# Performance work log

Measured on AMD Instinct MI355X. Metric: run time of the kernel, lower is better.

The kernel has to match this reference:

```python
import jax, jax.numpy as jnp
import numpy as np

B, S, DIM = 2, 2048, 2048
N_HEADS, N_KV_HEADS = 16, 4
HEAD_DIM = DIM // N_HEADS  # 128
N_REP = N_HEADS // N_KV_HEADS  # 4
ROPE_THETA = 10000.0


def setup_inputs() -> dict:
    key = jax.random.key(0)
    ks = jax.random.split(key, 6)
    x = jax.random.normal(ks[0], (B, S, DIM), dtype=jnp.float32)
    # torch nn.Linear weights are [out_features, in_features]
    sc = 0.02
    wq = jax.random.normal(ks[1], (N_HEADS * HEAD_DIM, DIM), dtype=jnp.float32) * sc
    wk = jax.random.normal(ks[2], (N_KV_HEADS * HEAD_DIM, DIM), dtype=jnp.float32) * sc
    wv = jax.random.normal(ks[3], (N_KV_HEADS * HEAD_DIM, DIM), dtype=jnp.float32) * sc
    wo = jax.random.normal(ks[4], (DIM, N_HEADS * HEAD_DIM), dtype=jnp.float32) * sc
    # precomputed rotary table (freqs_cis in llama): [S, head_dim//2]
    inv_freq = 1.0 / (ROPE_THETA ** (jnp.arange(0, HEAD_DIM, 2, dtype=jnp.float32) / HEAD_DIM))
    t = jnp.arange(S, dtype=jnp.float32)
    freqs = jnp.outer(t, inv_freq)  # [S, head_dim//2]
    freqs_cos = jnp.cos(freqs)
    freqs_sin = jnp.sin(freqs)
    # additive causal mask as passed to SDPA (float, 0 on allowed, -inf-like elsewhere)
    causal = jnp.tril(jnp.ones((S, S), dtype=bool))
    mask = jnp.where(causal, 0.0, -1e9).astype(jnp.float32)
    return {"x": x, "wq": wq, "wk": wk, "wv": wv, "wo": wo,
            "freqs_cos": freqs_cos, "freqs_sin": freqs_sin, "mask": mask}


def _apply_rope(t, cos, sin):
    # t: [B, S, H, D]; cos/sin: [S, D//2] -> complex multiply on adjacent pairs
    tr = t.reshape(*t.shape[:-1], -1, 2)  # [B,S,H,D/2,2]
    tre, tim = tr[..., 0], tr[..., 1]
    c = cos[None, :, None, :]
    s = sin[None, :, None, :]
    out_re = tre * c - tim * s
    out_im = tre * s + tim * c
    return jnp.stack([out_re, out_im], axis=-1).reshape(t.shape)


def reference(x, wq, wk, wv, wo, freqs_cos, freqs_sin, mask):
    Bx, Sx, _ = x.shape
    xq = (x @ wq.T).reshape(Bx, Sx, N_HEADS, HEAD_DIM)
    xk = (x @ wk.T).reshape(Bx, Sx, N_KV_HEADS, HEAD_DIM)
    xv = (x @ wv.T).reshape(Bx, Sx, N_KV_HEADS, HEAD_DIM)
    xq = _apply_rope(xq, freqs_cos, freqs_sin)
    xk = _apply_rope(xk, freqs_cos, freqs_sin)
    # repeat_kv for GQA: [B,S,KV,D] -> [B,S,KV*n_rep,D]
    keys = jnp.repeat(xk, N_REP, axis=2)
    values = jnp.repeat(xv, N_REP, axis=2)
    q = xq.transpose(0, 2, 1, 3)      # [B,H,S,D]
    k = keys.transpose(0, 2, 1, 3)
    v = values.transpose(0, 2, 1, 3)
    scale = 1.0 / jnp.sqrt(jnp.float32(HEAD_DIM))
    scores = jnp.einsum('bhqd,bhkd->bhqk', q, k) * scale + mask[None, None]
    attn = jax.nn.softmax(scores, axis=-1)
    out = jnp.einsum('bhqk,bhkd->bhqd', attn, v)
    out = out.transpose(0, 2, 1, 3).reshape(Bx, Sx, -1)
    return out @ wo.T
```

## Files before the change

kernel.cpp:

```cpp
#include <hip/hip_runtime.h>
#include <hip/hip_bf16.h>

#define B_   2
#define S_   2048
#define DIM_ 2048
#define NH   16
#define NKV  4
#define HD   128
#define QKVN 3072

typedef __attribute__((ext_vector_type(8)))  short  sv8;
typedef __attribute__((ext_vector_type(8)))  ushort usv8;
typedef __attribute__((ext_vector_type(4)))  float  fv4;
typedef __attribute__((ext_vector_type(16))) float  fv16;

__device__ __forceinline__ float fast_exp2(float x) {
  return __builtin_amdgcn_exp2f(x);
}

__device__ __forceinline__ ushort f2bf(float f) {
  __hip_bfloat16 h = __float2bfloat16(f);
  union { __hip_bfloat16 h; ushort u; } c; c.h = h; return c.u;
}
__device__ __forceinline__ float bf2f(ushort u) {
  union { unsigned int i; float f; } c; c.i = ((unsigned)u) << 16; return c.f;
}

__device__ __forceinline__ unsigned int cvtpk(float lo, float hi) {
  unsigned int r;
  asm("v_cvt_pk_bf16_f32 %0, %1, %2" : "=v"(r) : "v"(lo), "v"(hi));
  return r;
}
__device__ __forceinline__ unsigned int xhalf(unsigned int x) {
  return (unsigned int)__shfl_xor((int)x, 32, 64);
}

__device__ __forceinline__ void async16(const void* g, void* l) {
  __builtin_amdgcn_global_load_lds(
      (const __attribute__((address_space(1))) unsigned int*)g,
      (__attribute__((address_space(3))) unsigned int*)l, 16, 0, 0);
}

__global__ void cvt_kernel(const float* __restrict__ in, ushort* __restrict__ out, int n) {
  int i = (blockIdx.x * 256 + threadIdx.x) * 4;
  if (i >= n) return;
  fv4 v = *(const fv4*)(in + i);
  ushort4 o;
  o.x = f2bf(v[0]); o.y = f2bf(v[1]); o.z = f2bf(v[2]); o.w = f2bf(v[3]);
  *(ushort4*)(out + i) = o;
}

__global__ void rope_kernel(const ushort* __restrict__ raw, const float* __restrict__ fc,
                            const float* __restrict__ fs, ushort* __restrict__ out,
                            int heads, int rowstride, float scale) {
  int t = blockIdx.x * 256 + threadIdx.x;
  int grp = t & 15;
  int h   = (t >> 4) % heads;
  int s   = ((t >> 4) / heads) % S_;
  int b   = t / (16 * heads * S_);
  const ushort* src = raw + (size_t)(b * S_ + s) * rowstride + h * HD + grp * 8;
  sv8 v = *(const sv8*)src;
  fv4 c  = *(const fv4*)(fc + s * 64 + grp * 4);
  fv4 sn = *(const fv4*)(fs + s * 64 + grp * 4);
  sv8 o;
#pragma unroll
  for (int p = 0; p < 4; ++p) {
    float re = bf2f((ushort)v[2 * p]);
    float im = bf2f((ushort)v[2 * p + 1]);
    float orr = (re * c[p] - im * sn[p]) * scale;
    float oi  = (re * sn[p] + im * c[p]) * scale;
    o[2 * p]     = (short)f2bf(orr);
    o[2 * p + 1] = (short)f2bf(oi);
  }
  ushort* dst = out + ((size_t)(b * heads + h) * S_ + s) * HD + grp * 8;
  *(sv8*)dst = o;
}

__global__ __launch_bounds__(256) void vtrans_kernel(const ushort* __restrict__ vraw,
                                                     ushort* __restrict__ vt, int rowstride) {
  __shared__ ushort tile[128][136];
  int blk = blockIdx.x;
  int st  = blk & 15;
  int kvb = blk >> 4;
  int kv  = kvb & 3;
  int b   = kvb >> 2;
  int s0  = st << 7;
#pragma unroll
  for (int it = 0; it < 8; ++it) {
    int t = it * 256 + threadIdx.x;
    int srow = t >> 4;
    int d8 = (t & 15) * 8;
    usv8 v = *(const usv8*)(vraw + (size_t)(b * S_ + s0 + srow) * rowstride + kv * HD + d8);
#pragma unroll
    for (int j = 0; j < 8; ++j) tile[d8 + j][srow] = v[j];
  }
  __syncthreads();
#pragma unroll
  for (int it = 0; it < 8; ++it) {
    int t = it * 256 + threadIdx.x;
    int d = t >> 4;
    int s8 = (t & 15) * 8;
    usv8 o;
#pragma unroll
    for (int j = 0; j < 8; ++j) o[j] = tile[d][s8 + j];
    *(usv8*)(vt + ((size_t)(b * NKV + kv) * HD + d) * S_ + s0 + s8) = o;
  }
}

template <typename OutT>
__global__ __launch_bounds__(256) void gemm_bt(const ushort* __restrict__ A,
                                               const ushort* __restrict__ Bm,
                                               OutT* __restrict__ C,
                                               int M, int N, int K) {
  __shared__ ushort As[128 * 64];
  __shared__ ushort Bs[128 * 64];
  int nb = N >> 7;
  int bx = blockIdx.x % nb;
  int by = blockIdx.x / nb;
  int m0 = by << 7, n0 = bx << 7;
  int lane = threadIdx.x & 63, w = threadIdx.x >> 6;
  int l15 = lane & 15, lg = lane >> 4;
  int wm = (w >> 1) * 64, wn = (w & 1) * 64;

  const ushort* aSrc[4]; const ushort* bSrc[4];
  ushort* aDst[4]; ushort* bDst[4];
#pragma unroll
  for (int it = 0; it < 4; ++it) {
    int lin = it * 4096 + w * 1024 + lane * 16;
    int row = lin >> 7;
    int cb  = (lin & 127) ^ ((row & 7) << 4);
    aSrc[it] = A  + (size_t)(m0 + row) * K + (cb >> 1);
    bSrc[it] = Bm + (size_t)(n0 + row) * K + (cb >> 1);
    aDst[it] = As + ((it * 4096 + w * 1024) >> 1);
    bDst[it] = Bs + ((it * 4096 + w * 1024) >> 1);
  }

  fv4 acc[4][4] = {};

  for (int kt = 0; kt < K; kt += 64) {
#pragma unroll
    for (int it = 0; it < 4; ++it) async16(aSrc[it] + kt, aDst[it]);
#pragma unroll
    for (int it = 0; it < 4; ++it) async16(bSrc[it] + kt, bDst[it]);
    __syncthreads();
#pragma unroll
    for (int kk = 0; kk < 2; ++kk) {
      sv8 af[4], bfr[4];
#pragma unroll
      for (int i = 0; i < 4; ++i) {
        int row = wm + i * 16 + l15;
        int byt = row * 128 + ((kk * 64 + (lg << 4)) ^ ((row & 7) << 4));
        af[i] = *(const sv8*)((const char*)As + byt);
      }
#pragma unroll
      for (int j = 0; j < 4; ++j) {
        int row = wn + j * 16 + l15;
        int byt = row * 128 + ((kk * 64 + (lg << 4)) ^ ((row & 7) << 4));
        bfr[j] = *(const sv8*)((const char*)Bs + byt);
      }
#pragma unroll
      for (int i = 0; i < 4; ++i)
#pragma unroll
        for (int j = 0; j < 4; ++j)
          acc[i][j] = __builtin_amdgcn_mfma_f32_16x16x32_bf16(af[i], bfr[j], acc[i][j], 0, 0, 0);
    }
    __syncthreads();
  }

#pragma unroll
  for (int i = 0; i < 4; ++i)
#pragma unroll
    for (int j = 0; j < 4; ++j)
#pragma unroll
      for (int r = 0; r < 4; ++r) {
        int row = m0 + wm + i * 16 + (lg << 2) + r;
        int col = n0 + wn + j * 16 + l15;
        if constexpr (sizeof(OutT) == 2) C[(size_t)row * N + col] = (OutT)f2bf(acc[i][j][r]);
        else                             C[(size_t)row * N + col] = (OutT)acc[i][j][r];
      }
}

__global__ __launch_bounds__(256, 2) void attn_kernel(const ushort* __restrict__ Q,
                                                      const ushort* __restrict__ Kr,
                                                      const ushort* __restrict__ Vt,
                                                      ushort* __restrict__ O) {
  __shared__ ushort Ks[2][64 * 128];
  __shared__ ushort Vs[2][128 * 64];

  int blk = blockIdx.x;
  int bh  = blk & 31;
  int idx = blk >> 5;
  int qt  = (idx & 1) ? (idx >> 1) : (15 - (idx >> 1));
  int h   = bh & 15;
  int b   = bh >> 4;
  int kv  = h >> 2;
  int q0  = qt << 7;
  int lane = threadIdx.x & 63, w = threadIdx.x >> 6;
  int l31 = lane & 31, hh = lane >> 5;
  int qrow_w = q0 + w * 32;
  int myq    = qrow_w + l31;

  const ushort* Qbase = Q  + (size_t)(b * NH  + h ) * S_ * HD;
  const ushort* Kbase = Kr + (size_t)(b * NKV + kv) * S_ * HD;
  const ushort* Vbase = Vt + (size_t)(b * NKV + kv) * HD * S_;

  sv8 qf[8];
#pragma unroll
  for (int kk = 0; kk < 8; ++kk)
    qf[kk] = *(const sv8*)(Qbase + (size_t)myq * HD + kk * 16 + hh * 8);

  const ushort* kSrc[4]; ushort* kDst[4];
  const ushort* vSrc[4]; ushort* vDst[4];
#pragma unroll
  for (int it = 0; it < 4; ++it) {
    int lin = it * 4096 + w * 1024 + lane * 16;
    { int row = lin >> 8; int cb = (lin & 255) ^ ((row & 7) << 4);
      kSrc[it] = Kbase + (size_t)row * HD + (cb >> 1);
      kDst[it] = Ks[0] + ((it * 4096 + w * 1024) >> 1); }
    { int row = lin >> 7; int cb = (lin & 127) ^ ((row & 7) << 4);
      vSrc[it] = Vbase + (size_t)row * S_ + (cb >> 1);
      vDst[it] = Vs[0] + ((it * 4096 + w * 1024) >> 1); }
  }

  fv16 oacc[4] = {};
  float mrun = -1e30f, lrun = 0.f;

  int nkt = (q0 >> 6) + 2;

#pragma unroll
  for (int it = 0; it < 4; ++it) async16(kSrc[it], kDst[it]);
#pragma unroll
  for (int it = 0; it < 4; ++it) async16(vSrc[it], vDst[it]);

  for (int kt = 0; kt < nkt; ++kt) {
    int cur = kt & 1, nxt = cur ^ 1;
    __syncthreads();
    if (kt + 1 < nkt) {
      size_t k0n = (size_t)(kt + 1) << 6;
#pragma unroll
      for (int it = 0; it < 4; ++it) async16(kSrc[it] + k0n * HD, kDst[it] + nxt * (64 * 128));
#pragma unroll
      for (int it = 0; it < 4; ++it) async16(vSrc[it] + k0n,      vDst[it] + nxt * (128 * 64));
    }
    const char* KsC = (const char*)Ks[cur];
    const char* VsC = (const char*)Vs[cur];
    int k0 = kt << 6;

    fv16 sacc[2] = {};
    __builtin_amdgcn_s_setprio(1);
#pragma unroll
    for (int kk = 0; kk < 8; ++kk) {
      int cb = kk * 32 + hh * 16;
      int r0 = l31, r1 = 32 + l31;
      sv8 kf0 = *(const sv8*)(KsC + r0 * 256 + (cb ^ ((r0 & 7) << 4)));
      sv8 kf1 = *(const sv8*)(KsC + r1 * 256 + (cb ^ ((r1 & 7) << 4)));
      sacc[0] = __builtin_amdgcn_mfma_f32_32x32x16_bf16(kf0, qf[kk], sacc[0], 0, 0, 0);
      sacc[1] = __builtin_amdgcn_mfma_f32_32x32x16_bf16(kf1, qf[kk], sacc[1], 0, 0, 0);
    }
    __builtin_amdgcn_s_setprio(0);

    if (k0 + 63 > qrow_w) {
      int thr = myq - k0 - 4 * hh;
#pragma unroll
      for (int t = 0; t < 2; ++t)
#pragma unroll
        for (int r = 0; r < 16; ++r) {
          int kp = t * 32 + (r & 3) + 8 * (r >> 2);
          if (kp > thr) sacc[t][r] = -1e30f;
        }
    }

    float tmax = sacc[0][0];
#pragma unroll
    for (int t = 0; t < 2; ++t)
#pragma unroll
      for (int r = 0; r < 16; ++r) tmax = fmaxf(tmax, sacc[t][r]);
    tmax = fmaxf(tmax, __shfl_xor(tmax, 32, 64));

    if (__any(tmax > mrun + 8.0f)) {
      float mnew = fmaxf(mrun, tmax);
      float esc  = fast_exp2(mrun - mnew);
      lrun *= esc;
      float er[16];
#pragma unroll
      for (int r = 0; r < 16; ++r) er[r] = __shfl(esc, (r & 3) + 8 * (r >> 2) + 4 * hh, 64);
#pragma unroll
      for (int d0 = 0; d0 < 4; ++d0)
#pragma unroll
        for (int r = 0; r < 16; ++r) oacc[d0][r] *= er[r];
      mrun = mnew;
    }

    float psum = 0.f;
#pragma unroll
    for (int t = 0; t < 2; ++t)
#pragma unroll
      for (int r = 0; r < 16; ++r) {
        float p = fast_exp2(sacc[t][r] - mrun);
        sacc[t][r] = p;
        psum += p;
      }
    psum += __shfl_xor(psum, 32, 64);
    lrun += psum;

    union Frag { unsigned int u[4]; sv8 v; } pa[4];
#pragma unroll
    for (int t = 0; t < 2; ++t)
#pragma unroll
      for (int half = 0; half < 2; ++half) {
        int cb = half * 8;
        unsigned int a0 = cvtpk(sacc[t][cb + 0], sacc[t][cb + 1]);
        unsigned int a1 = cvtpk(sacc[t][cb + 2], sacc[t][cb + 3]);
        unsigned int b0 = cvtpk(sacc[t][cb + 4], sacc[t][cb + 5]);
        unsigned int b1 = cvtpk(sacc[t][cb + 6], sacc[t][cb + 7]);
        unsigned int a0p = xhalf(a0), a1p = xhalf(a1);
        unsigned int b0p = xhalf(b0), b1p = xhalf(b1);
        pa[2 * t + half].u[0] = hh ? b0p : a0;
        pa[2 * t + half].u[1] = hh ? b1p : a1;
        pa[2 * t + half].u[2] = hh ? b0  : a0p;
        pa[2 * t + half].u[3] = hh ? b1  : a1p;
      }

    __builtin_amdgcn_s_setprio(1);
#pragma unroll
    for (int ks = 0; ks < 4; ++ks) {
      int cb = ks * 32 + hh * 16;
#pragma unroll
      for (int d0 = 0; d0 < 4; ++d0) {
        int row = d0 * 32 + l31;
        sv8 vf = *(const sv8*)(VsC + row * 128 + (cb ^ ((row & 7) << 4)));
        oacc[d0] = __builtin_amdgcn_mfma_f32_32x32x16_bf16(pa[ks].v, vf, oacc[d0], 0, 0, 0);
      }
    }
    __builtin_amdgcn_s_setprio(0);
  }

  float inv = 1.0f / lrun;
  float ir[16];
#pragma unroll
  for (int r = 0; r < 16; ++r) ir[r] = __shfl(inv, (r & 3) + 8 * (r >> 2) + 4 * hh, 64);
#pragma unroll
  for (int r = 0; r < 16; ++r) {
    int q = qrow_w + (r & 3) + 8 * (r >> 2) + 4 * hh;
#pragma unroll
    for (int d0 = 0; d0 < 4; ++d0) {
      int d = d0 * 32 + l31;
      O[(size_t)(b * S_ + q) * DIM_ + h * HD + d] = f2bf(oacc[d0][r] * ir[r]);
    }
  }
}

extern "C" void kernel_launch(void* const* d_in, const int* in_sizes, int n_in,
                              void* d_out, int out_size, void* d_ws, size_t ws_size,
                              hipStream_t stream) {
  const float* x  = (const float*)d_in[0];
  const float* wq = (const float*)d_in[1];
  const float* wk = (const float*)d_in[2];
  const float* wv = (const float*)d_in[3];
  const float* wo = (const float*)d_in[4];
  const float* fc = (const float*)d_in[5];
  const float* fs = (const float*)d_in[6];
  float* out = (float*)d_out;

  char* ws = (char*)d_ws;
  size_t off = 0;
  auto alloc = [&](size_t bytes) -> ushort* {
    ushort* p = (ushort*)(ws + off);
    off += (bytes + 255) & ~(size_t)255;
    return p;
  };
  ushort* xb    = alloc((size_t)B_ * S_ * DIM_ * 2);
  ushort* wqkvb = alloc((size_t)QKVN * DIM_ * 2);
  ushort* wob   = alloc((size_t)DIM_ * DIM_ * 2);
  ushort* qkvr  = alloc((size_t)B_ * S_ * QKVN * 2);
  ushort* qr    = alloc((size_t)B_ * S_ * DIM_ * 2);
  ushort* kr    = alloc((size_t)B_ * S_ * NKV * HD * 2);
  ushort* vtb   = alloc((size_t)B_ * S_ * NKV * HD * 2);
  ushort* obf   = alloc((size_t)B_ * S_ * DIM_ * 2);
  (void)ws_size; (void)n_in; (void)in_sizes; (void)out_size;

  cvt_kernel<<<(B_ * S_ * DIM_) / 1024, 256, 0, stream>>>(x,  xb, B_ * S_ * DIM_);
  cvt_kernel<<<(DIM_ * DIM_) / 1024,     256, 0, stream>>>(wq, wqkvb,                 DIM_ * DIM_);
  cvt_kernel<<<(NKV * HD * DIM_) / 1024, 256, 0, stream>>>(wk, wqkvb + 2048 * DIM_,   NKV * HD * DIM_);
  cvt_kernel<<<(NKV * HD * DIM_) / 1024, 256, 0, stream>>>(wv, wqkvb + 2560 * DIM_,   NKV * HD * DIM_);
  cvt_kernel<<<(DIM_ * DIM_) / 1024,     256, 0, stream>>>(wo, wob, DIM_ * DIM_);

  gemm_bt<ushort><<<(B_ * S_ / 128) * (QKVN / 128), 256, 0, stream>>>(xb, wqkvb, qkvr,
                                                                     B_ * S_, QKVN, DIM_);

  const float qscale = 0.08838834764831845f * 1.4426950408889634f;
  rope_kernel<<<(B_ * S_ * NH  * 16) / 256, 256, 0, stream>>>(qkvr,        fc, fs, qr, NH,  QKVN, qscale);
  rope_kernel<<<(B_ * S_ * NKV * 16) / 256, 256, 0, stream>>>(qkvr + 2048, fc, fs, kr, NKV, QKVN, 1.0f);
  vtrans_kernel<<<B_ * NKV * (S_ / 128), 256, 0, stream>>>(qkvr + 2560, vtb, QKVN);

  attn_kernel<<<B_ * NH * (S_ / 128), 256, 0, stream>>>(qr, kr, vtb, obf);

  gemm_bt<float><<<(B_ * S_ / 128) * (DIM_ / 128), 256, 0, stream>>>(obf, wob, out, B_ * S_, DIM_, DIM_);
}
```

Before: 220.1 us.

## Pair causal query tiles per attention block for balanced work

Each attention block now handles two query tiles in sequence, a short tile qt and its mirror 15-qt. Every block therefore does the same total number of KV iterations, and the grid is halved to 256 blocks. The max and sum reductions over the score accumulators are also rewritten as balanced trees to shorten dependency chains. In exchange there are fewer blocks to fill the CUs (256 blocks of 256 threads at 2 per CU), and a block's runtime is the serial sum of both passes.

```diff
diff --git a/kernel.cpp b/kernel.cpp
--- a/kernel.cpp
+++ b/kernel.cpp
@@ -33,6 +33,21 @@
 }
 __device__ __forceinline__ unsigned int xhalf(unsigned int x) {
   return (unsigned int)__shfl_xor((int)x, 32, 64);
+}
+
+__device__ __forceinline__ float tmax16(const fv16& v) {
+  float a = fmaxf(fmaxf(v[0], v[1]),  fmaxf(v[2], v[3]));
+  float b = fmaxf(fmaxf(v[4], v[5]),  fmaxf(v[6], v[7]));
+  float c = fmaxf(fmaxf(v[8], v[9]),  fmaxf(v[10], v[11]));
+  float d = fmaxf(fmaxf(v[12], v[13]), fmaxf(v[14], v[15]));
+  return fmaxf(fmaxf(a, b), fmaxf(c, d));
+}
+__device__ __forceinline__ float tsum16(const fv16& v) {
+  float a = (v[0] + v[1]) + (v[2] + v[3]);
+  float b = (v[4] + v[5]) + (v[6] + v[7]);
+  float c = (v[8] + v[9]) + (v[10] + v[11]);
+  float d = (v[12] + v[13]) + (v[14] + v[15]);
+  return (a + b) + (c + d);
 }
 
 __device__ __forceinline__ void async16(const void* g, void* l) {
@@ -189,25 +204,16 @@
 
   int blk = blockIdx.x;
   int bh  = blk & 31;
-  int idx = blk >> 5;
-  int qt  = (idx & 1) ? (idx >> 1) : (15 - (idx >> 1));
+  int pr  = blk >> 5;
   int h   = bh & 15;
   int b   = bh >> 4;
   int kv  = h >> 2;
-  int q0  = qt << 7;
   int lane = threadIdx.x & 63, w = threadIdx.x >> 6;
   int l31 = lane & 31, hh = lane >> 5;
-  int qrow_w = q0 + w * 32;
-  int myq    = qrow_w + l31;
 
   const ushort* Qbase = Q  + (size_t)(b * NH  + h ) * S_ * HD;
   const ushort* Kbase = Kr + (size_t)(b * NKV + kv) * S_ * HD;
   const ushort* Vbase = Vt + (size_t)(b * NKV + kv) * HD * S_;
-
-  sv8 qf[8];
-#pragma unroll
-  for (int kk = 0; kk < 8; ++kk)
-    qf[kk] = *(const sv8*)(Qbase + (size_t)myq * HD + kk * 16 + hh * 8);
 
   const ushort* kSrc[4]; ushort* kDst[4];
   const ushort* vSrc[4]; ushort* vDst[4];
@@ -222,130 +228,136 @@
       vDst[it] = Vs[0] + ((it * 4096 + w * 1024) >> 1); }
   }
 
-  fv16 oacc[4] = {};
-  float mrun = -1e30f, lrun = 0.f;
-
-  int nkt = (q0 >> 6) + 2;
-
-#pragma unroll
-  for (int it = 0; it < 4; ++it) async16(kSrc[it], kDst[it]);
-#pragma unroll
-  for (int it = 0; it < 4; ++it) async16(vSrc[it], vDst[it]);
-
-  for (int kt = 0; kt < nkt; ++kt) {
-    int cur = kt & 1, nxt = cur ^ 1;
-    __syncthreads();
-    if (kt + 1 < nkt) {
-      size_t k0n = (size_t)(kt + 1) << 6;
-#pragma unroll
-      for (int it = 0; it < 4; ++it) async16(kSrc[it] + k0n * HD, kDst[it] + nxt * (64 * 128));
-#pragma unroll
-      for (int it = 0; it < 4; ++it) async16(vSrc[it] + k0n,      vDst[it] + nxt * (128 * 64));
+  for (int pass = 0; pass < 2; ++pass) {
+    int qt = pass ? (15 - pr) : pr;
+    int q0 = qt << 7;
+    int qrow_w = q0 + w * 32;
+    int myq    = qrow_w + l31;
+
+    sv8 qf[8];
+#pragma unroll
+    for (int kk = 0; kk < 8; ++kk)
+      qf[kk] = *(const sv8*)(Qbase + (size_t)myq * HD + kk * 16 + hh * 8);
+
+    fv16 oacc[4] = {};
+    float mrun = -1e30f, lrun = 0.f;
+
+    int nkt = (q0 >> 6) + 2;
+
+    if (pass) __syncthreads();
+
+#pragma unroll
+    for (int it = 0; it < 4; ++it) async16(kSrc[it], kDst[it]);
+#pragma unroll
+    for (int it = 0; it < 4; ++it) async16(vSrc[it], vDst[it]);
+
+    for (int kt = 0; kt < nkt; ++kt) {
+      int cur = kt & 1, nxt = cur ^ 1;
+      __syncthreads();
+      if (kt + 1 < nkt) {
+        size_t k0n = (size_t)(kt + 1) << 6;
+#pragma unroll
+        for (int it = 0; it < 4; ++it) async16(kSrc[it] + k0n * HD, kDst[it] + nxt * (64 * 128));
+#pragma unroll
+        for (int it = 0; it < 4; ++it) async16(vSrc[it] + k0n,      vDst[it] + nxt * (128 * 64));
+      }
+      const char* KsC = (const char*)Ks[cur];
+      const char* VsC = (const char*)Vs[cur];
+      int k0 = kt << 6;
+
+      fv16 sacc[2] = {};
+      __builtin_amdgcn_s_setprio(1);
+#pragma unroll
+      for (int kk = 0; kk < 8; ++kk) {
+        int cb = kk * 32 + hh * 16;
+        int r0 = l31, r1 = 32 + l31;
+        sv8 kf0 = *(const sv8*)(KsC + r0 * 256 + (cb ^ ((r0 & 7) << 4)));
+        sv8 kf1 = *(const sv8*)(KsC + r1 * 256 + (cb ^ ((r1 & 7) << 4)));
+        sacc[0] = __builtin_amdgcn_mfma_f32_32x32x16_bf16(kf0, qf[kk], sacc[0], 0, 0, 0);
+        sacc[1] = __builtin_amdgcn_mfma_f32_32x32x16_bf16(kf1, qf[kk], sacc[1], 0, 0, 0);
+      }
+      __builtin_amdgcn_s_setprio(0);
+
+      if (k0 + 63 > qrow_w) {
+        int thr = myq - k0 - 4 * hh;
+#pragma unroll
+        for (int t = 0; t < 2; ++t)
+#pragma unroll
+          for (int r = 0; r < 16; ++r) {
+            int kp = t * 32 + (r & 3) + 8 * (r >> 2);
+            if (kp > thr) sacc[t][r] = -1e30f;
+          }
+      }
+
+      float tmax = fmaxf(tmax16(sacc[0]), tmax16(sacc[1]));
+      tmax = fmaxf(tmax, __shfl_xor(tmax, 32, 64));
+
+      if (__any(tmax > mrun + 8.0f)) {
+        float mnew = fmaxf(mrun, tmax);
+        float esc  = fast_exp2(mrun - mnew);
+        lrun *= esc;
+        float er[16];
+#pragma unroll
+        for (int r = 0; r < 16; ++r) er[r] = __shfl(esc, (r & 3) + 8 * (r >> 2) + 4 * hh, 64);
+#pragma unroll
+        for (int d0 = 0; d0 < 4; ++d0)
+#pragma unroll
+          for (int r = 0; r < 16; ++r) oacc[d0][r] *= er[r];
+        mrun = mnew;
+      }
+
+#pragma unroll
+      for (int t = 0; t < 2; ++t)
+#pragma unroll
+        for (int r = 0; r < 16; ++r) sacc[t][r] = fast_exp2(sacc[t][r] - mrun);
+      float psum = tsum16(sacc[0]) + tsum16(sacc[1]);
+      psum += __shfl_xor(psum, 32, 64);
+      lrun += psum;
+
+      union Frag { unsigned int u[4]; sv8 v; } pa[4];
+#pragma unroll
+      for (int t = 0; t < 2; ++t)
+#pragma unroll
+        for (int half = 0; half < 2; ++half) {
+          int cb = half * 8;
+          unsigned int a0 = cvtpk(sacc[t][cb + 0], sacc[t][cb + 1]);
+          unsigned int a1 = cvtpk(sacc[t][cb + 2], sacc[t][cb + 3]);
+          unsigned int b0 = cvtpk(sacc[t][cb + 4], sacc[t][cb + 5]);
+          unsigned int b1 = cvtpk(sacc[t][cb + 6], sacc[t][cb + 7]);
+          unsigned int a0p = xhalf(a0), a1p = xhalf(a1);
+          unsigned int b0p = xhalf(b0), b1p = xhalf(b1);
+          pa[2 * t + half].u[0] = hh ? b0p : a0;
+          pa[2 * t + half].u[1] = hh ? b1p : a1;
+          pa[2 * t + half].u[2] = hh ? b0  : a0p;
+          pa[2 * t + half].u[3] = hh ? b1  : a1p;
+        }
+
+      __builtin_amdgcn_s_setprio(1);
+#pragma unroll
+      for (int ks = 0; ks < 4; ++ks) {
+        int cb = ks * 32 + hh * 16;
+#pragma unroll
+        for (int d0 = 0; d0 < 4; ++d0) {
+          int row = d0 * 32 + l31;
+          sv8 vf = *(const sv8*)(VsC + row * 128 + (cb ^ ((row & 7) << 4)));
+          oacc[d0] = __builtin_amdgcn_mfma_f32_32x32x16_bf16(pa[ks].v, vf, oacc[d0], 0, 0, 0);
+        }
+      }
+      __builtin_amdgcn_s_setprio(0);
     }
-    const char* KsC = (const char*)Ks[cur];
-    const char* VsC = (const char*)Vs[cur];
-    int k0 = kt << 6;
-
-    fv16 sacc[2] = {};
-    __builtin_amdgcn_s_setprio(1);
-#pragma unroll
-    for (int kk = 0; kk < 8; ++kk) {
-      int cb = kk * 32 + hh * 16;
-      int r0 = l31, r1 = 32 + l31;
-      sv8 kf0 = *(const sv8*)(KsC + r0 * 256 + (cb ^ ((r0 & 7) << 4)));
-      sv8 kf1 = *(const sv8*)(KsC + r1 * 256 + (cb ^ ((r1 & 7) << 4)));
-      sacc[0] = __builtin_amdgcn_mfma_f32_32x32x16_bf16(kf0, qf[kk], sacc[0], 0, 0, 0);
-      sacc[1] = __builtin_amdgcn_mfma_f32_32x32x16_bf16(kf1, qf[kk], sacc[1], 0, 0, 0);
-    }
-    __builtin_amdgcn_s_setprio(0);
-
-    if (k0 + 63 > qrow_w) {
-      int thr = myq - k0 - 4 * hh;
-#pragma unroll
-      for (int t = 0; t < 2; ++t)
-#pragma unroll
-        for (int r = 0; r < 16; ++r) {
-          int kp = t * 32 + (r & 3) + 8 * (r >> 2);
-          if (kp > thr) sacc[t][r] = -1e30f;
-        }
-    }
-
-    float tmax = sacc[0][0];
-#pragma unroll
-    for (int t = 0; t < 2; ++t)
-#pragma unroll
-      for (int r = 0; r < 16; ++r) tmax = fmaxf(tmax, sacc[t][r]);
-    tmax = fmaxf(tmax, __shfl_xor(tmax, 32, 64));
-
-    if (__any(tmax > mrun + 8.0f)) {
-      float mnew = fmaxf(mrun, tmax);
-      float esc  = fast_exp2(mrun - mnew);
-      lrun *= esc;
-      float er[16];
-#pragma unroll
-      for (int r = 0; r < 16; ++r) er[r] = __shfl(esc, (r & 3) + 8 * (r >> 2) + 4 * hh, 64);
-#pragma unroll
-      for (int d0 = 0; d0 < 4; ++d0)
-#pragma unroll
-        for (int r = 0; r < 16; ++r) oacc[d0][r] *= er[r];
-      mrun = mnew;
-    }
-
-    float psum = 0.f;
-#pragma unroll
-    for (int t = 0; t < 2; ++t)
-#pragma unroll
-      for (int r = 0; r < 16; ++r) {
-        float p = fast_exp2(sacc[t][r] - mrun);
-        sacc[t][r] = p;
-        psum += p;
-      }
-    psum += __shfl_xor(psum, 32, 64);
-    lrun += psum;
-
-    union Frag { unsigned int u[4]; sv8 v; } pa[4];
-#pragma unroll
-    for (int t = 0; t < 2; ++t)
-#pragma unroll
-      for (int half = 0; half < 2; ++half) {
-        int cb = half * 8;
-        unsigned int a0 = cvtpk(sacc[t][cb + 0], sacc[t][cb + 1]);
-        unsigned int a1 = cvtpk(sacc[t][cb + 2], sacc[t][cb + 3]);
-        unsigned int b0 = cvtpk(sacc[t][cb + 4], sacc[t][cb + 5]);
-        unsigned int b1 = cvtpk(sacc[t][cb + 6], sacc[t][cb + 7]);
-        unsigned int a0p = xhalf(a0), a1p = xhalf(a1);
-        unsigned int b0p = xhalf(b0), b1p = xhalf(b1);
-        pa[2 * t + half].u[0] = hh ? b0p : a0;
-        pa[2 * t + half].u[1] = hh ? b1p : a1;
-        pa[2 * t + half].u[2] = hh ? b0  : a0p;
-        pa[2 * t + half].u[3] = hh ? b1  : a1p;
-      }
-
-    __builtin_amdgcn_s_setprio(1);
-#pragma unroll
-    for (int ks = 0; ks < 4; ++ks) {
-      int cb = ks * 32 + hh * 16;
+
+    float inv = 1.0f / lrun;
+    float ir[16];
+#pragma unroll
+    for (int r = 0; r < 16; ++r) ir[r] = __shfl(inv, (r & 3) + 8 * (r >> 2) + 4 * hh, 64);
+#pragma unroll
+    for (int r = 0; r < 16; ++r) {
+      int q = qrow_w + (r & 3) + 8 * (r >> 2) + 4 * hh;
 #pragma unroll
       for (int d0 = 0; d0 < 4; ++d0) {
-        int row = d0 * 32 + l31;
-        sv8 vf = *(const sv8*)(VsC + row * 128 + (cb ^ ((row & 7) << 4)));
-        oacc[d0] = __builtin_amdgcn_mfma_f32_32x32x16_bf16(pa[ks].v, vf, oacc[d0], 0, 0, 0);
-      }
-    }
-    __builtin_amdgcn_s_setprio(0);
-  }
-
-  float inv = 1.0f / lrun;
-  float ir[16];
-#pragma unroll
-  for (int r = 0; r < 16; ++r) ir[r] = __shfl(inv, (r & 3) + 8 * (r >> 2) + 4 * hh, 64);
-#pragma unroll
-  for (int r = 0; r < 16; ++r) {
-    int q = qrow_w + (r & 3) + 8 * (r >> 2) + 4 * hh;
-#pragma unroll
-    for (int d0 = 0; d0 < 4; ++d0) {
-      int d = d0 * 32 + l31;
-      O[(size_t)(b * S_ + q) * DIM_ + h * HD + d] = f2bf(oacc[d0][r] * ir[r]);
+        int d = d0 * 32 + l31;
+        O[(size_t)(b * S_ + q) * DIM_ + h * HD + d] = f2bf(oacc[d0][r] * ir[r]);
+      }
     }
   }
 }
@@ -393,7 +405,7 @@
   rope_kernel<<<(B_ * S_ * NKV * 16) / 256, 256, 0, stream>>>(qkvr + 2048, fc, fs, kr, NKV, QKVN, 1.0f);
   vtrans_kernel<<<B_ * NKV * (S_ / 128), 256, 0, stream>>>(qkvr + 2560, vtb, QKVN);
 
-  attn_kernel<<<B_ * NH * (S_ / 128), 256, 0, stream>>>(qr, kr, vtb, obf);
+  attn_kernel<<<B_ * NH * 8, 256, 0, stream>>>(qr, kr, vtb, obf);
 
   gemm_bt<float><<<(B_ * S_ / 128) * (DIM_ / 128), 256, 0, stream>>>(obf, wob, out, B_ * S_, DIM_, DIM_);
 }
```

New measurement: 216.7 us. About the same (-1.6%).
